# Performance work log

Hardware: AMD Instinct MI355X
Metric: run time of the kernel (lower is better)

## Reference

```python
import jax, jax.numpy as jnp
import numpy as np

K_HOPS = 3  # spektral TAGConv default
BN_EPS = 1e-3  # keras BatchNormalization default epsilon


def _propagate(x, edge_src, edge_dst, edge_weight, n_nodes):
    # y[dst] += w * x[src]  (sparse adjacency @ x)
    msg = x[edge_src] * edge_weight[:, None]
    return jax.ops.segment_sum(msg, edge_dst, num_segments=n_nodes)


def _tag_conv(x, edge_src, edge_dst, edge_weight, W, b):
    n = x.shape[0]
    hops = [x]
    h = x
    for _ in range(K_HOPS):
        h = _propagate(h, edge_src, edge_dst, edge_weight, n)
        hops.append(h)
    # concat hops along features then dense combine: [N, F*(K+1)] @ [F*(K+1), C]
    return jnp.concatenate(hops, axis=-1) @ W + b


def setup_inputs() -> dict:
    key = jax.random.key(0)
    ks = jax.random.split(key, 6)
    N, F, E, H, L = 20000, 2000, 640000, 128, 15
    x = jax.random.normal(ks[0], (N, F), dtype=jnp.float32)
    edge_src = jax.random.randint(ks[1], (E,), 0, N, dtype=jnp.int32)
    edge_dst = jax.random.randint(ks[2], (E,), 0, N, dtype=jnp.int32)
    # normalized adjacency weights, roughly 1/avg_degree scale
    edge_weight = jax.random.uniform(ks[3], (E,), dtype=jnp.float32) / 32.0
    W1 = jax.random.normal(ks[4], (F * (K_HOPS + 1), H), dtype=jnp.float32) * (1.0 / np.sqrt(F * (K_HOPS + 1)))
    b1 = jnp.zeros((H,), dtype=jnp.float32)
    gamma = jnp.ones((H,), dtype=jnp.float32)
    beta = jnp.zeros((H,), dtype=jnp.float32)
    moving_mean = jnp.zeros((H,), dtype=jnp.float32)
    moving_var = jnp.ones((H,), dtype=jnp.float32)
    W2 = jax.random.normal(ks[5], (H * (K_HOPS + 1), L), dtype=jnp.float32) * (1.0 / np.sqrt(H * (K_HOPS + 1)))
    b2 = jnp.zeros((L,), dtype=jnp.float32)
    return {"x": x, "edge_src": edge_src, "edge_dst": edge_dst, "edge_weight": edge_weight,
            "W1": W1, "b1": b1, "gamma": gamma, "beta": beta,
            "moving_mean": moving_mean, "moving_var": moving_var, "W2": W2, "b2": b2}


def reference(x, edge_src, edge_dst, edge_weight, W1, b1, gamma, beta,
              moving_mean, moving_var, W2, b2):
    # training=False: Dropout is identity, BN uses moving statistics
    h = _tag_conv(x, edge_src, edge_dst, edge_weight, W1, b1)
    h = (h - moving_mean) * jax.lax.rsqrt(moving_var + BN_EPS) * gamma + beta
    h = jax.nn.relu(h)
    z = _tag_conv(h, edge_src, edge_dst, edge_weight, W2, b2)
    return z
```

## Files before the change

### kernel.cpp

```cpp
#include <hip/hip_runtime.h>
#include <cstdint>
#include <cstddef>

#define N_NODES 20000
#define F_IN    2000
#define H_DIM   128
#define L_DIM   15
#define K_PAD   2048
#define M_PAD   20096
#define N1      512
#define BM      128
#define BN      128
#define BK      32

typedef __attribute__((ext_vector_type(4))) float f32x4;
typedef __attribute__((ext_vector_type(8))) short s16x8;
typedef __attribute__((ext_vector_type(8))) unsigned short u16x8;

__device__ __forceinline__ unsigned short f2bf(float f) {
  unsigned int u = __float_as_uint(f);
  u += 0x7fff + ((u >> 16) & 1);
  return (unsigned short)(u >> 16);
}

__global__ __launch_bounds__(256) void k_cvt_x(const float* __restrict__ x,
                                               unsigned short* __restrict__ xb) {
  unsigned int t = blockIdx.x * 256u + threadIdx.x;
  unsigned int row = t >> 8;
  unsigned int colB = (t & 255u) * 8u;
  u16x8 o = {0, 0, 0, 0, 0, 0, 0, 0};
  if (row < N_NODES && colB < F_IN) {
    const float4 a = *(const float4*)(x + (size_t)row * F_IN + colB);
    const float4 b = *(const float4*)(x + (size_t)row * F_IN + colB + 4);
    o[0] = f2bf(a.x); o[1] = f2bf(a.y); o[2] = f2bf(a.z); o[3] = f2bf(a.w);
    o[4] = f2bf(b.x); o[5] = f2bf(b.y); o[6] = f2bf(b.z); o[7] = f2bf(b.w);
  }
  *(u16x8*)(xb + (size_t)t * 8) = o;
}

__global__ __launch_bounds__(256) void k_cvt_w1(const float* __restrict__ W1,
                                                unsigned short* __restrict__ bt) {
  unsigned int t = blockIdx.x * 256u + threadIdx.x;
  unsigned int n = t >> 8;
  unsigned int kB = (t & 255u) * 8u;
  u16x8 o = {0, 0, 0, 0, 0, 0, 0, 0};
  if (kB < F_IN) {
    unsigned int hop = n >> 7, c = n & 127;
    const float* p = W1 + (size_t)(hop * F_IN + kB) * H_DIM + c;
#pragma unroll
    for (int q = 0; q < 8; ++q) o[q] = f2bf(p[(size_t)q * H_DIM]);
  }
  *(u16x8*)(bt + (size_t)t * 8) = o;
}

__global__ __launch_bounds__(256) void k_gemm1(const unsigned short* __restrict__ A,
                                               const unsigned short* __restrict__ B,
                                               float* __restrict__ C) {
  __shared__ unsigned short As[BM * BK];
  __shared__ unsigned short Bs[BN * BK];
  const int tid  = threadIdx.x;
  const int lane = tid & 63;
  const int wave = tid >> 6;
  const int wm = (wave >> 1) * 64;
  const int wn = (wave & 1) * 64;
  const int rowA0 = blockIdx.y * BM;
  const int colB0 = blockIdx.x * BN;
  const int quad = lane >> 4;
  const int l15  = lane & 15;
  f32x4 acc[4][4] = {};

  for (int kt = 0; kt < K_PAD; kt += BK) {
#pragma unroll
    for (int r = 0; r < 2; ++r) {
      int c = r * 256 + tid;
      int row = c >> 2;
      int kc = (c & 3) * 8;
      const unsigned short* ga = A + (size_t)(rowA0 + row) * K_PAD + kt + kc;
      __builtin_amdgcn_global_load_lds((const __attribute__((address_space(1))) void*)ga,
                                       (__attribute__((address_space(3))) void*)(As + c * 8),
                                       16, 0, 0);
      const unsigned short* gb = B + (size_t)(colB0 + row) * K_PAD + kt + kc;
      __builtin_amdgcn_global_load_lds((const __attribute__((address_space(1))) void*)gb,
                                       (__attribute__((address_space(3))) void*)(Bs + c * 8),
                                       16, 0, 0);
    }
    __syncthreads();
    s16x8 af[4], bfr[4];
#pragma unroll
    for (int i = 0; i < 4; ++i)
      af[i] = *(const s16x8*)(As + (wm + i * 16 + l15) * BK + quad * 8);
#pragma unroll
    for (int j = 0; j < 4; ++j)
      bfr[j] = *(const s16x8*)(Bs + (wn + j * 16 + l15) * BK + quad * 8);
#pragma unroll
    for (int i = 0; i < 4; ++i)
#pragma unroll
      for (int j = 0; j < 4; ++j)
        acc[i][j] = __builtin_amdgcn_mfma_f32_16x16x32_bf16(af[i], bfr[j], acc[i][j], 0, 0, 0);
    __syncthreads();
  }

#pragma unroll
  for (int i = 0; i < 4; ++i) {
    int row0 = rowA0 + wm + i * 16 + quad * 4;
#pragma unroll
    for (int j = 0; j < 4; ++j) {
      int col = colB0 + wn + j * 16 + l15;
#pragma unroll
      for (int r = 0; r < 4; ++r) {
        int row = row0 + r;
        if (row < N_NODES) C[(size_t)row * N1 + col] = acc[i][j][r];
      }
    }
  }
}

__global__ __launch_bounds__(256) void k_hist(const int* __restrict__ dst,
                                              int* __restrict__ deg, int E) {
  int i = blockIdx.x * 256 + threadIdx.x;
  int e = i * 4;
  if (e + 4 <= E) {
    int4 d4 = *(const int4*)(dst + e);
    atomicAdd(&deg[d4.x], 1); atomicAdd(&deg[d4.y], 1);
    atomicAdd(&deg[d4.z], 1); atomicAdd(&deg[d4.w], 1);
  } else {
    for (; e < E; ++e) atomicAdd(&deg[dst[e]], 1);
  }
}

__global__ __launch_bounds__(1024) void k_scan(const int* __restrict__ deg,
                                               int* __restrict__ rowStart,
                                               int* __restrict__ cursor) {
  __shared__ int sums[1024];
  const int t = threadIdx.x;
  const int chunk = (N_NODES + 1023) / 1024;
  int lo = t * chunk;
  int hi = lo + chunk; if (hi > N_NODES) hi = N_NODES;
  int s = 0;
  for (int i = lo; i < hi; ++i) s += deg[i];
  sums[t] = s;
  __syncthreads();
  for (int off = 1; off < 1024; off <<= 1) {
    int v = sums[t];
    int u = (t >= off) ? sums[t - off] : 0;
    __syncthreads();
    sums[t] = v + u;
    __syncthreads();
  }
  int run = sums[t] - s;
  for (int i = lo; i < hi; ++i) {
    rowStart[i] = run; cursor[i] = run; run += deg[i];
  }
  if (t == 1023) rowStart[N_NODES] = run;
}

__global__ __launch_bounds__(256) void k_scatter(const int* __restrict__ src,
                                                 const int* __restrict__ dst,
                                                 const float* __restrict__ w,
                                                 int* cursor,
                                                 int2* __restrict__ eSW, int E) {
  int e = blockIdx.x * 256 + threadIdx.x;
  if (e >= E) return;
  int p = atomicAdd(&cursor[dst[e]], 1);
  eSW[p] = make_int2(src[e], __float_as_int(w[e]));
}

__global__ __launch_bounds__(256) void k_prop128(const int* __restrict__ rowStart,
    const int2* __restrict__ eSW,
    const float* __restrict__ in, int inStride, int inOff,
    const float* __restrict__ addv, int addStride, int addOff,
    float* __restrict__ out,
    const float* __restrict__ b1, const float* __restrict__ gamma,
    const float* __restrict__ beta, const float* __restrict__ mean,
    const float* __restrict__ var, int doBN) {
  const int lane = threadIdx.x & 63;
  const int d = blockIdx.x * 4 + (threadIdx.x >> 6);
  const int s0 = rowStart[d], s1 = rowStart[d + 1];
  const int c2 = lane * 2;
  float2 acc = make_float2(0.f, 0.f);
  int j = s0;
  for (; j + 4 <= s1; j += 4) {
    int2 e0 = eSW[j], e1 = eSW[j + 1], e2 = eSW[j + 2], e3 = eSW[j + 3];
    float2 v0 = *(const float2*)(in + (size_t)e0.x * inStride + inOff + c2);
    float2 v1 = *(const float2*)(in + (size_t)e1.x * inStride + inOff + c2);
    float2 v2 = *(const float2*)(in + (size_t)e2.x * inStride + inOff + c2);
    float2 v3 = *(const float2*)(in + (size_t)e3.x * inStride + inOff + c2);
    float w0 = __int_as_float(e0.y), w1 = __int_as_float(e1.y);
    float w2 = __int_as_float(e2.y), w3 = __int_as_float(e3.y);
    acc.x = fmaf(w0, v0.x, acc.x); acc.y = fmaf(w0, v0.y, acc.y);
    acc.x = fmaf(w1, v1.x, acc.x); acc.y = fmaf(w1, v1.y, acc.y);
    acc.x = fmaf(w2, v2.x, acc.x); acc.y = fmaf(w2, v2.y, acc.y);
    acc.x = fmaf(w3, v3.x, acc.x); acc.y = fmaf(w3, v3.y, acc.y);
  }
  for (; j < s1; ++j) {
    int2 e = eSW[j];
    float2 v = *(const float2*)(in + (size_t)e.x * inStride + inOff + c2);
    float w = __int_as_float(e.y);
    acc.x = fmaf(w, v.x, acc.x); acc.y = fmaf(w, v.y, acc.y);
  }
  float2 av = *(const float2*)(addv + (size_t)d * addStride + addOff + c2);
  float r0 = av.x + acc.x, r1 = av.y + acc.y;
  if (doBN) {
    float2 bb = *(const float2*)(b1 + c2);
    float2 gg = *(const float2*)(gamma + c2);
    float2 be = *(const float2*)(beta + c2);
    float2 mm = *(const float2*)(mean + c2);
    float2 vv = *(const float2*)(var + c2);
    r0 = (r0 + bb.x - mm.x) * rsqrtf(vv.x + 1e-3f) * gg.x + be.x;
    r1 = (r1 + bb.y - mm.y) * rsqrtf(vv.y + 1e-3f) * gg.y + be.y;
    r0 = r0 > 0.f ? r0 : 0.f;
    r1 = r1 > 0.f ? r1 : 0.f;
  }
  *(float2*)(out + (size_t)d * H_DIM + c2) = make_float2(r0, r1);
}

__global__ __launch_bounds__(256) void k_gemm2(const float* __restrict__ Hh,
                                               const float* __restrict__ W2,
                                               float* __restrict__ Y2) {
  __shared__ float w2s[512 * 15];
  for (int i = threadIdx.x; i < 512 * 15; i += 256) w2s[i] = W2[i];
  __syncthreads();
  const int c = threadIdx.x & 63;
  const int d = blockIdx.x * 4 + (threadIdx.x >> 6);
  if (c >= 60 || d >= N_NODES) return;
  const int hop = c / 15, j = c % 15;
  const float4* hr4 = (const float4*)(Hh + (size_t)d * H_DIM);
  float acc = 0.f;
#pragma unroll 8
  for (int k4 = 0; k4 < 32; ++k4) {
    float4 h = hr4[k4];
    const float* wp = w2s + ((hop << 7) + k4 * 4) * 15 + j;
    acc = fmaf(h.x, wp[0],  acc);
    acc = fmaf(h.y, wp[15], acc);
    acc = fmaf(h.z, wp[30], acc);
    acc = fmaf(h.w, wp[45], acc);
  }
  Y2[(size_t)d * 60 + c] = acc;
}

__global__ __launch_bounds__(256) void k_prop15(const int* __restrict__ rowStart,
    const int2* __restrict__ eSW,
    const float* __restrict__ in, int inStride, int inOff,
    const float* __restrict__ addv, int addStride, int addOff,
    const float* __restrict__ bias, float* __restrict__ out) {
  const int f = threadIdx.x & 15;
  const int d = blockIdx.x * 16 + (threadIdx.x >> 4);
  if (f >= 15) return;
  const int s0 = rowStart[d], s1 = rowStart[d + 1];
  float acc = 0.f;
  int j = s0;
  for (; j + 4 <= s1; j += 4) {
    int2 e0 = eSW[j], e1 = eSW[j + 1], e2 = eSW[j + 2], e3 = eSW[j + 3];
    float v0 = in[(size_t)e0.x * inStride + inOff + f];
    float v1 = in[(size_t)e1.x * inStride + inOff + f];
    float v2 = in[(size_t)e2.x * inStride + inOff + f];
    float v3 = in[(size_t)e3.x * inStride + inOff + f];
    acc = fmaf(__int_as_float(e0.y), v0, acc);
    acc = fmaf(__int_as_float(e1.y), v1, acc);
    acc = fmaf(__int_as_float(e2.y), v2, acc);
    acc = fmaf(__int_as_float(e3.y), v3, acc);
  }
  for (; j < s1; ++j) {
    int2 e = eSW[j];
    acc = fmaf(__int_as_float(e.y), in[(size_t)e.x * inStride + inOff + f], acc);
  }
  float b = bias ? bias[f] : 0.f;
  out[(size_t)d * 15 + f] = addv[(size_t)d * addStride + addOff + f] + acc + b;
}

extern "C" void kernel_launch(void* const* d_in, const int* in_sizes, int n_in,
                              void* d_out, int out_size, void* d_ws, size_t ws_size,
                              hipStream_t stream) {
  const float* x     = (const float*)d_in[0];
  const int*   esrc  = (const int*)d_in[1];
  const int*   edst  = (const int*)d_in[2];
  const float* ew    = (const float*)d_in[3];
  const float* W1    = (const float*)d_in[4];
  const float* b1    = (const float*)d_in[5];
  const float* gamma = (const float*)d_in[6];
  const float* beta  = (const float*)d_in[7];
  const float* mmean = (const float*)d_in[8];
  const float* mvar  = (const float*)d_in[9];
  const float* W2    = (const float*)d_in[10];
  const float* b2    = (const float*)d_in[11];
  const int E = in_sizes[1];
  char* ws = (char*)d_ws;

  unsigned short* xb  = (unsigned short*)(ws);
  unsigned short* w1r = (unsigned short*)(ws + 82313216);
  float* Y        = (float*)(ws + 84410368);
  int*   deg      = (int*)(ws + 125370368);
  int*   rowStart = (int*)(ws + 125450496);
  int*   cursor   = (int*)(ws + 125530624);
  int2*  eSW      = (int2*)(ws + 125610752);
  float* P   = (float*)(ws);
  float* Q   = (float*)(ws + 10240000);
  float* Hb  = (float*)(ws + 20480000);
  float* Y2  = (float*)(ws + 30720000);
  float* zP  = (float*)(ws + 35520000);
  float* zQ  = (float*)(ws + 36720000);
  float* zout = (float*)d_out;

  hipMemsetAsync(deg, 0, N_NODES * sizeof(int), stream);
  k_hist<<<(E / 4 + 255) / 256 + 1, 256, 0, stream>>>(edst, deg, E);
  k_scan<<<1, 1024, 0, stream>>>(deg, rowStart, cursor);
  k_scatter<<<(E + 255) / 256, 256, 0, stream>>>(esrc, edst, ew, cursor, eSW, E);

  k_cvt_x<<<(M_PAD * K_PAD / 8) / 256, 256, 0, stream>>>(x, xb);
  k_cvt_w1<<<(N1 * K_PAD / 8) / 256, 256, 0, stream>>>(W1, w1r);
  dim3 g1(N1 / BN, M_PAD / BM);
  k_gemm1<<<g1, 256, 0, stream>>>(xb, w1r, Y);

  k_prop128<<<N_NODES / 4, 256, 0, stream>>>(rowStart, eSW, Y, N1, 3 * H_DIM, Y, N1, 2 * H_DIM, P,
                                             b1, gamma, beta, mmean, mvar, 0);
  k_prop128<<<N_NODES / 4, 256, 0, stream>>>(rowStart, eSW, P, H_DIM, 0, Y, N1, 1 * H_DIM, Q,
                                             b1, gamma, beta, mmean, mvar, 0);
  k_prop128<<<N_NODES / 4, 256, 0, stream>>>(rowStart, eSW, Q, H_DIM, 0, Y, N1, 0, Hb,
                                             b1, gamma, beta, mmean, mvar, 1);

  k_gemm2<<<N_NODES / 4, 256, 0, stream>>>(Hb, W2, Y2);
  k_prop15<<<N_NODES / 16, 256, 0, stream>>>(rowStart, eSW, Y2, 60, 45, Y2, 60, 30, nullptr, zP);
  k_prop15<<<N_NODES / 16, 256, 0, stream>>>(rowStart, eSW, zP, 15, 0, Y2, 60, 15, nullptr, zQ);
  k_prop15<<<N_NODES / 16, 256, 0, stream>>>(rowStart, eSW, zQ, 15, 0, Y2, 60, 0, b2, zout);
}
```

Before: 640.7 us.

## Transpose W1 via LDS, swizzle GEMM block order, unroll propagation by eight

The W1 conversion kernel now reads W1 with coalesced float4 loads, transposes it to bf16 through a padded LDS tile, and writes contiguous 16-byte rows, replacing strided scalar reads. The GEMM moves from a 2D grid to a 1D grid of 640 blocks, remapped into groups of 8 row tiles by 4 column tiles so that blocks running together share A and B tiles in cache; blocks past the last row tile exit early. The 128-wide propagation kernel gains an 8-edge unrolled loop that issues more independent gathers per iteration, at the cost of more registers.

Result: no change. 633.6 us (-1.1%).

```diff
diff --git a/kernel.cpp b/kernel.cpp
--- a/kernel.cpp
+++ b/kernel.cpp
@@ -40,17 +40,34 @@
 
 __global__ __launch_bounds__(256) void k_cvt_w1(const float* __restrict__ W1,
                                                 unsigned short* __restrict__ bt) {
-  unsigned int t = blockIdx.x * 256u + threadIdx.x;
-  unsigned int n = t >> 8;
-  unsigned int kB = (t & 255u) * 8u;
-  u16x8 o = {0, 0, 0, 0, 0, 0, 0, 0};
-  if (kB < F_IN) {
-    unsigned int hop = n >> 7, c = n & 127;
-    const float* p = W1 + (size_t)(hop * F_IN + kB) * H_DIM + c;
-#pragma unroll
-    for (int q = 0; q < 8; ++q) o[q] = f2bf(p[(size_t)q * H_DIM]);
-  }
-  *(u16x8*)(bt + (size_t)t * 8) = o;
+  __shared__ unsigned short tile[128 * 67];
+  const int hop = blockIdx.x >> 5;
+  const int k0  = (blockIdx.x & 31) * 64;
+  const int t = threadIdx.x;
+#pragma unroll
+  for (int it = 0; it < 8; ++it) {
+    int f4 = it * 256 + t;
+    int r  = f4 >> 5;
+    int c4 = f4 & 31;
+    int k = k0 + r;
+    float4 v = make_float4(0.f, 0.f, 0.f, 0.f);
+    if (k < F_IN) v = *(const float4*)(W1 + (size_t)(hop * F_IN + k) * H_DIM + c4 * 4);
+    tile[(c4 * 4 + 0) * 67 + r] = f2bf(v.x);
+    tile[(c4 * 4 + 1) * 67 + r] = f2bf(v.y);
+    tile[(c4 * 4 + 2) * 67 + r] = f2bf(v.z);
+    tile[(c4 * 4 + 3) * 67 + r] = f2bf(v.w);
+  }
+  __syncthreads();
+  const int c = t >> 1, kh = (t & 1) * 32;
+  unsigned short* dst = bt + (size_t)(hop * 128 + c) * K_PAD + k0 + kh;
+  const unsigned short* srcp = tile + c * 67 + kh;
+#pragma unroll
+  for (int q = 0; q < 4; ++q) {
+    u16x8 o;
+#pragma unroll
+    for (int e = 0; e < 8; ++e) o[e] = srcp[q * 8 + e];
+    *(u16x8*)(dst + q * 8) = o;
+  }
 }
 
 __global__ __launch_bounds__(256) void k_gemm1(const unsigned short* __restrict__ A,
@@ -58,13 +75,17 @@
                                                float* __restrict__ C) {
   __shared__ unsigned short As[BM * BK];
   __shared__ unsigned short Bs[BN * BK];
+  const int b = blockIdx.x;
+  const int i_tile = (b & 7) + 8 * (b >> 5);
+  const int j_tile = (b >> 3) & 3;
+  if (i_tile >= M_PAD / BM) return;
+  const int rowA0 = i_tile * BM;
+  const int colB0 = j_tile * BN;
   const int tid  = threadIdx.x;
   const int lane = tid & 63;
   const int wave = tid >> 6;
   const int wm = (wave >> 1) * 64;
   const int wn = (wave & 1) * 64;
-  const int rowA0 = blockIdx.y * BM;
-  const int colB0 = blockIdx.x * BN;
   const int quad = lane >> 4;
   const int l15  = lane & 15;
   f32x4 acc[4][4] = {};
@@ -179,6 +200,30 @@
   const int c2 = lane * 2;
   float2 acc = make_float2(0.f, 0.f);
   int j = s0;
+  for (; j + 8 <= s1; j += 8) {
+    int2 e0 = eSW[j],     e1 = eSW[j + 1], e2 = eSW[j + 2], e3 = eSW[j + 3];
+    int2 e4 = eSW[j + 4], e5 = eSW[j + 5], e6 = eSW[j + 6], e7 = eSW[j + 7];
+    float2 v0 = *(const float2*)(in + (size_t)e0.x * inStride + inOff + c2);
+    float2 v1 = *(const float2*)(in + (size_t)e1.x * inStride + inOff + c2);
+    float2 v2 = *(const float2*)(in + (size_t)e2.x * inStride + inOff + c2);
+    float2 v3 = *(const float2*)(in + (size_t)e3.x * inStride + inOff + c2);
+    float2 v4 = *(const float2*)(in + (size_t)e4.x * inStride + inOff + c2);
+    float2 v5 = *(const float2*)(in + (size_t)e5.x * inStride + inOff + c2);
+    float2 v6 = *(const float2*)(in + (size_t)e6.x * inStride + inOff + c2);
+    float2 v7 = *(const float2*)(in + (size_t)e7.x * inStride + inOff + c2);
+    float w0 = __int_as_float(e0.y), w1 = __int_as_float(e1.y);
+    float w2 = __int_as_float(e2.y), w3 = __int_as_float(e3.y);
+    float w4 = __int_as_float(e4.y), w5 = __int_as_float(e5.y);
+    float w6 = __int_as_float(e6.y), w7 = __int_as_float(e7.y);
+    acc.x = fmaf(w0, v0.x, acc.x); acc.y = fmaf(w0, v0.y, acc.y);
+    acc.x = fmaf(w1, v1.x, acc.x); acc.y = fmaf(w1, v1.y, acc.y);
+    acc.x = fmaf(w2, v2.x, acc.x); acc.y = fmaf(w2, v2.y, acc.y);
+    acc.x = fmaf(w3, v3.x, acc.x); acc.y = fmaf(w3, v3.y, acc.y);
+    acc.x = fmaf(w4, v4.x, acc.x); acc.y = fmaf(w4, v4.y, acc.y);
+    acc.x = fmaf(w5, v5.x, acc.x); acc.y = fmaf(w5, v5.y, acc.y);
+    acc.x = fmaf(w6, v6.x, acc.x); acc.y = fmaf(w6, v6.y, acc.y);
+    acc.x = fmaf(w7, v7.x, acc.x); acc.y = fmaf(w7, v7.y, acc.y);
+  }
   for (; j + 4 <= s1; j += 4) {
     int2 e0 = eSW[j], e1 = eSW[j + 1], e2 = eSW[j + 2], e3 = eSW[j + 3];
     float2 v0 = *(const float2*)(in + (size_t)e0.x * inStride + inOff + c2);
@@ -307,9 +352,8 @@
   k_scatter<<<(E + 255) / 256, 256, 0, stream>>>(esrc, edst, ew, cursor, eSW, E);
 
   k_cvt_x<<<(M_PAD * K_PAD / 8) / 256, 256, 0, stream>>>(x, xb);
-  k_cvt_w1<<<(N1 * K_PAD / 8) / 256, 256, 0, stream>>>(W1, w1r);
-  dim3 g1(N1 / BN, M_PAD / BM);
-  k_gemm1<<<g1, 256, 0, stream>>>(xb, w1r, Y);
+  k_cvt_w1<<<128, 256, 0, stream>>>(W1, w1r);
+  k_gemm1<<<640, 256, 0, stream>>>(xb, w1r, Y);
 
   k_prop128<<<N_NODES / 4, 256, 0, stream>>>(rowStart, eSW, Y, N1, 3 * H_DIM, Y, N1, 2 * H_DIM, P,
                                              b1, gamma, beta, mmean, mvar, 0);
```
